# Kernel tuning notes

Hardware: AMD Instinct MI355X
Metric: run time of the kernel (lower is better)

Reference implementation:

```python
import jax, jax.numpy as jnp
import numpy as np

N_CLASSES = 12
IMG_SIZE = 512
BATCH = 8

CURV_MAX = jnp.array([1.2261, 1.1558, 1.1161, 1.1195, 2.7202, 2.3714,
                      1.7055, 3.2717, 2.6716, 5.0418, 0.4293], dtype=jnp.float32)


def setup_inputs() -> dict:
    key = jax.random.key(0)
    soft_anatomy = jax.random.normal(key, (BATCH, N_CLASSES, IMG_SIZE, IMG_SIZE), dtype=jnp.float32)
    return {"soft_anatomy": soft_anatomy}


def reference(soft_anatomy):
    nc1 = N_CLASSES - 1  # 11 layer channels
    pred_mask = soft_anatomy[:, :nc1]                      # [B, 11, H, W]
    sm = jax.nn.softmax(pred_mask, axis=2)                 # softmax over height (dim 2)
    lsm = jax.nn.log_softmax(pred_mask, axis=2)
    B, C, H, W = sm.shape

    # position mask: row index broadcast over width/channels
    pos = jnp.arange(H, dtype=sm.dtype)[None, None, :, None]  # [1,1,H,1]

    # expected layer position per column: [B, 11, W]
    layer_positions = jnp.sum(sm * pos, axis=2)

    # std deviations around layer positions: [B, 11, W]
    std_deviations = jnp.sqrt(
        jnp.sum(sm * (pos - layer_positions[:, :, None, :]) ** 2, axis=2))

    # topology violations between adjacent layers: [B, 10, W]
    topology_violations = jax.nn.relu(layer_positions[:, :-1] - layer_positions[:, 1:])

    # neighbour (continuity) diff along width: [B, 11, W-1]
    continuity_violations = jnp.abs(
        (jnp.roll(layer_positions, 1, axis=2) - layer_positions)[..., 1:])

    # curvature via depthwise conv1d with sobel [-1,0..0,1] and laplace [1,0..0,-2,0..0,1]
    # (kernel length 11, replicate pad 5 -> same width). torch conv1d is cross-correlation:
    #   first[w]  = -x[w] + x[w+10]
    #   second[w] =  x[w] - 2*x[w+5] + x[w+10]
    PAD = 5
    lpp = jnp.pad(layer_positions, ((0, 0), (0, 0), (PAD, PAD)), mode='edge')
    first_order = lpp[..., 10:] - lpp[..., :-10]
    second_order = lpp[..., :-10] - 2.0 * lpp[..., 5:-5] + lpp[..., 10:]
    curvature = second_order / jnp.power(1.0 + first_order ** 2, 1.5)
    curvature_diffs = jnp.abs(curvature) - CURV_MAX[None, :, None]  # curv_max broadcast over W

    # topological_engine_1d: new[i] = max(new[i-1], lp[i]) == cumulative max over class dim
    correct_layer_positions = jax.lax.cummax(layer_positions, axis=1)

    # cumulative mask: ones channel + cumsum over height -> [B, 12, H, W]
    cum = jnp.cumsum(sm, axis=2)
    ones = jnp.ones((B, 1, H, W), dtype=sm.dtype)
    cm = jnp.concatenate([ones, cum], axis=1)

    # topological_engine_2d: y[idx] = relu(c[idx] + y[idx-1] - 1), idx = 2..n_classes-1
    def step(carry, c):
        y = jax.nn.relu(c + carry - 1.0)
        return y, y

    _, ys = jax.lax.scan(step, cm[:, 1], jnp.moveaxis(cm[:, 2:], 1, 0))
    top_correct = jnp.concatenate([cm[:, :2], jnp.moveaxis(ys, 0, 1)], axis=1)  # [B,12,H,W]

    # separate_masks: forward diff in place; last channel unchanged
    clean_masks = jnp.concatenate(
        [top_correct[:, :-1] - top_correct[:, 1:], top_correct[:, -1:]], axis=1)

    return (lsm, correct_layer_positions, clean_masks,
            std_deviations, topology_violations, continuity_violations, curvature_diffs)
```

## Files before the change

### kernel.cpp

```cpp
#include <hip/hip_runtime.h>

#define BB 8
#define NC 12
#define NC1 11
#define HH 512
#define WW 512
#define NG 64
#define GH 8

static constexpr size_t CH = (size_t)HH * WW;

static constexpr size_t OFF_LSM   = 0;
static constexpr size_t OFF_CLP   = (size_t)BB * NC1 * CH;
static constexpr size_t OFF_CLEAN = OFF_CLP + (size_t)BB * NC1 * WW;
static constexpr size_t OFF_STD   = OFF_CLEAN + (size_t)BB * NC * CH;
static constexpr size_t OFF_TOPO  = OFF_STD + (size_t)BB * NC1 * WW;
static constexpr size_t OFF_CONT  = OFF_TOPO + (size_t)BB * (NC1 - 1) * WW;
static constexpr size_t OFF_CURV  = OFF_CONT + (size_t)BB * NC1 * (WW - 1);

static constexpr size_t WS_BASE = 0;
static constexpr size_t WS_INV  = WS_BASE + (size_t)BB * NC1 * NG * WW;
static constexpr size_t WS_LOG  = WS_INV + (size_t)BB * NC1 * WW;
static constexpr size_t WS_LP   = WS_LOG + (size_t)BB * NC1 * WW;

__global__ __launch_bounds__(256) void ka_stats(const float* __restrict__ in,
                                                float* __restrict__ ws,
                                                float* __restrict__ out) {
    const int tx = threadIdx.x & 63;
    const int ty = threadIdx.x >> 6;
    const int wt = blockIdx.x;
    const int c  = blockIdx.y;
    const int b  = blockIdx.z;
    const int w  = wt * 128 + tx * 2;
    const int bc = b * NC1 + c;

    __shared__ float lE[NG][128];
    __shared__ float lP[4][128];
    __shared__ float lQ[4][128];

    const float* p = in + (size_t)(b * NC + c) * CH + (size_t)(ty * 128) * WW + w;
    float Px = 0.f, Py = 0.f, Qx = 0.f, Qy = 0.f;
    for (int gl = 0; gl < 16; ++gl) {
        float Ex = 0.f, Ey = 0.f, P8x = 0.f, P8y = 0.f, Q8x = 0.f, Q8y = 0.f;
        const float hbase = (float)(ty * 128 + gl * 8);
#pragma unroll
        for (int i = 0; i < GH; ++i) {
            float2 x = *(const float2*)(p + (size_t)(gl * 8 + i) * WW);
            float ex = expf(x.x), ey = expf(x.y);
            float h = hbase + (float)i;
            Ex += ex; Ey += ey;
            P8x += h * ex; P8y += h * ey;
            Q8x += h * h * ex; Q8y += h * h * ey;
        }
        *(float2*)&lE[ty * 16 + gl][tx * 2] = make_float2(Ex, Ey);
        Px += P8x; Py += P8y;
        Qx += Q8x; Qy += Q8y;
    }
    *(float2*)&lP[ty][tx * 2] = make_float2(Px, Py);
    *(float2*)&lQ[ty][tx * 2] = make_float2(Qx, Qy);
    __syncthreads();
    if (ty != 0) return;

    float Sx = 0.f, Sy = 0.f;
#pragma unroll
    for (int g = 0; g < NG; ++g) {
        float2 e = *(const float2*)&lE[g][tx * 2];
        Sx += e.x; Sy += e.y;
    }
    const float invx = 1.f / Sx, invy = 1.f / Sy;
    float rx = 0.f, ry = 0.f;
    float* bp = ws + WS_BASE + (size_t)bc * NG * WW + w;
#pragma unroll
    for (int g = 0; g < NG; ++g) {
        *(float2*)(bp + (size_t)g * WW) = make_float2(rx * invx, ry * invy);
        float2 e = *(const float2*)&lE[g][tx * 2];
        rx += e.x; ry += e.y;
    }
    float Ptx = lP[0][tx*2] + lP[1][tx*2] + lP[2][tx*2] + lP[3][tx*2];
    float Pty = lP[0][tx*2+1] + lP[1][tx*2+1] + lP[2][tx*2+1] + lP[3][tx*2+1];
    float Qtx = lQ[0][tx*2] + lQ[1][tx*2] + lQ[2][tx*2] + lQ[3][tx*2];
    float Qty = lQ[0][tx*2+1] + lQ[1][tx*2+1] + lQ[2][tx*2+1] + lQ[3][tx*2+1];
    float lpx = Ptx * invx, lpy = Pty * invy;
    float vx = Qtx * invx - lpx * lpx; if (vx < 0.f) vx = 0.f;
    float vy = Qty * invy - lpy * lpy; if (vy < 0.f) vy = 0.f;

    const size_t o = (size_t)bc * WW + w;
    *(float2*)(ws + WS_INV + o) = make_float2(invx, invy);
    *(float2*)(ws + WS_LOG + o) = make_float2(logf(Sx), logf(Sy));
    *(float2*)(ws + WS_LP + o)  = make_float2(lpx, lpy);
    *(float2*)(out + OFF_STD + o) = make_float2(sqrtf(vx), sqrtf(vy));
}

__global__ __launch_bounds__(256) void kb_emit(const float* __restrict__ in,
                                               const float* __restrict__ ws,
                                               float* __restrict__ out) {
    const int t = threadIdx.x;
    const int g = blockIdx.x;
    const int b = blockIdx.y;
    const int w = t * 2;

    float2 cum[NC1], inv[NC1], lgs[NC1];
#pragma unroll
    for (int c = 0; c < NC1; ++c) {
        const size_t bc = (size_t)(b * NC1 + c);
        cum[c] = *(const float2*)(ws + WS_BASE + (bc * NG + g) * WW + w);
        inv[c] = *(const float2*)(ws + WS_INV + bc * WW + w);
        lgs[c] = *(const float2*)(ws + WS_LOG + bc * WW + w);
    }
    const float* ip  = in + (size_t)b * NC * CH + (size_t)(g * GH) * WW + w;
    float* lsm = out + OFF_LSM + (size_t)b * NC1 * CH + (size_t)(g * GH) * WW + w;
    float* cln = out + OFF_CLEAN + (size_t)b * NC * CH + (size_t)(g * GH) * WW + w;

    for (int i = 0; i < GH; ++i) {
        const size_t ho = (size_t)i * WW;
        float2 x[NC1];
#pragma unroll
        for (int c = 0; c < NC1; ++c)
            x[c] = *(const float2*)(ip + (size_t)c * CH + ho);
#pragma unroll
        for (int c = 0; c < NC1; ++c) {
            cum[c].x += expf(x[c].x) * inv[c].x;
            cum[c].y += expf(x[c].y) * inv[c].y;
            *(float2*)(lsm + (size_t)c * CH + ho) =
                make_float2(x[c].x - lgs[c].x, x[c].y - lgs[c].y);
        }
        float2 tc = cum[0];
        *(float2*)(cln + ho) = make_float2(1.f - tc.x, 1.f - tc.y);
#pragma unroll
        for (int k = 1; k < NC1; ++k) {
            float2 t2 = make_float2(fmaxf(cum[k].x + tc.x - 1.f, 0.f),
                                    fmaxf(cum[k].y + tc.y - 1.f, 0.f));
            *(float2*)(cln + (size_t)k * CH + ho) = make_float2(tc.x - t2.x, tc.y - t2.y);
            tc = t2;
        }
        *(float2*)(cln + (size_t)NC1 * CH + ho) = tc;
    }

    if (g != 0) return;
    const float CM[NC1] = {1.2261f, 1.1558f, 1.1161f, 1.1195f, 2.7202f, 2.3714f,
                           1.7055f, 3.2717f, 2.6716f, 5.0418f, 0.4293f};
    const float* lp = ws + WS_LP;
#pragma unroll
    for (int s = 0; s < 2; ++s) {
        const int wv = w + s;
        const int wm = (wv - 5 < 0) ? 0 : wv - 5;
        const int wp = (wv + 5 > WW - 1) ? WW - 1 : wv + 5;
        float m = 0.f, prev = 0.f;
        for (int c = 0; c < NC1; ++c) {
            const size_t rb = (size_t)(b * NC1 + c) * WW;
            const float lv = lp[rb + wv];
            m = (c == 0) ? lv : fmaxf(m, lv);
            out[OFF_CLP + rb + wv] = m;
            if (c > 0)
                out[OFF_TOPO + (size_t)(b * (NC1 - 1) + (c - 1)) * WW + wv] =
                    fmaxf(prev - lv, 0.f);
            prev = lv;
            if (wv < WW - 1) {
                const float nxt = lp[rb + wv + 1];
                out[OFF_CONT + (size_t)(b * NC1 + c) * (WW - 1) + wv] = fabsf(lv - nxt);
            }
            const float a  = lp[rb + wm];
            const float bb = lp[rb + wp];
            const float fo = bb - a;
            const float so = a - 2.f * lv + bb;
            const float bs = 1.f + fo * fo;
            out[OFF_CURV + rb + wv] = fabsf(so / (bs * sqrtf(bs))) - CM[c];
        }
    }
}

extern "C" void kernel_launch(void* const* d_in, const int* in_sizes, int n_in,
                              void* d_out, int out_size, void* d_ws, size_t ws_size,
                              hipStream_t stream) {
    const float* in = (const float*)d_in[0];
    float* out = (float*)d_out;
    float* ws = (float*)d_ws;

    hipLaunchKernelGGL(ka_stats, dim3(4, NC1, BB), dim3(256), 0, stream, in, ws, out);
    hipLaunchKernelGGL(kb_emit, dim3(NG, BB), dim3(256), 0, stream, in, ws, out);
}
```

Measured before the change: 83.54 us.

## Stage full column in LDS to emit log-softmax in stats pass, clean reads lsm

The stats kernel now loads an entire 512-row by 32-column tile into shared memory, computes the softmax stats, and writes log-softmax directly from LDS, so the input is read from global memory only once. The second kernel no longer reads the input. It reconstructs softmax as exp of the stored log-softmax and builds the clean masks from 32 chunk prefix offsets. This removes one full input read but adds a read-back of the lsm output, plus a 68KB LDS footprint per block that limits occupancy.

```diff
diff --git a/kernel.cpp b/kernel.cpp
--- a/kernel.cpp
+++ b/kernel.cpp
@@ -5,8 +5,10 @@
 #define NC1 11
 #define HH 512
 #define WW 512
-#define NG 64
-#define GH 8
+#define NCH 32
+#define HC 16
+#define WT 32
+#define XLD 34
 
 static constexpr size_t CH = (size_t)HH * WW;
 
@@ -19,153 +21,158 @@
 static constexpr size_t OFF_CURV  = OFF_CONT + (size_t)BB * NC1 * (WW - 1);
 
 static constexpr size_t WS_BASE = 0;
-static constexpr size_t WS_INV  = WS_BASE + (size_t)BB * NC1 * NG * WW;
-static constexpr size_t WS_LOG  = WS_INV + (size_t)BB * NC1 * WW;
-static constexpr size_t WS_LP   = WS_LOG + (size_t)BB * NC1 * WW;
+static constexpr size_t WS_LP   = WS_BASE + (size_t)BB * NC1 * NCH * WW;
 
-__global__ __launch_bounds__(256) void ka_stats(const float* __restrict__ in,
+__global__ __launch_bounds__(512) void ks_stats(const float* __restrict__ in,
                                                 float* __restrict__ ws,
                                                 float* __restrict__ out) {
-    const int tx = threadIdx.x & 63;
-    const int ty = threadIdx.x >> 6;
-    const int wt = blockIdx.x;
-    const int c  = blockIdx.y;
-    const int b  = blockIdx.z;
-    const int w  = wt * 128 + tx * 2;
+    const int t  = threadIdx.x;
+    const int wt = blockIdx.x, c = blockIdx.y, b = blockIdx.z;
     const int bc = b * NC1 + c;
+    const int w0 = wt * WT;
 
-    __shared__ float lE[NG][128];
-    __shared__ float lP[4][128];
-    __shared__ float lQ[4][128];
+    __shared__ float xs[HH][XLD];
+    __shared__ float cs[NCH][WT];
+    __shared__ float pP[16][WT];
+    __shared__ float pQ[16][WT];
+    __shared__ float lgS[WT];
 
-    const float* p = in + (size_t)(b * NC + c) * CH + (size_t)(ty * 128) * WW + w;
-    float Px = 0.f, Py = 0.f, Qx = 0.f, Qy = 0.f;
-    for (int gl = 0; gl < 16; ++gl) {
-        float Ex = 0.f, Ey = 0.f, P8x = 0.f, P8y = 0.f, Q8x = 0.f, Q8y = 0.f;
-        const float hbase = (float)(ty * 128 + gl * 8);
+    {
+        const int w2 = t & 15, r = t >> 4;
+        const float* p = in + (size_t)(b * NC + c) * CH + (size_t)r * WW + w0 + 2 * w2;
 #pragma unroll
-        for (int i = 0; i < GH; ++i) {
-            float2 x = *(const float2*)(p + (size_t)(gl * 8 + i) * WW);
-            float ex = expf(x.x), ey = expf(x.y);
-            float h = hbase + (float)i;
-            Ex += ex; Ey += ey;
-            P8x += h * ex; P8y += h * ey;
-            Q8x += h * h * ex; Q8y += h * h * ey;
+        for (int i = 0; i < 16; ++i) {
+            float2 v = *(const float2*)(p + (size_t)(i * 32) * WW);
+            xs[r + 32 * i][2 * w2]     = v.x;
+            xs[r + 32 * i][2 * w2 + 1] = v.y;
         }
-        *(float2*)&lE[ty * 16 + gl][tx * 2] = make_float2(Ex, Ey);
-        Px += P8x; Py += P8y;
-        Qx += Q8x; Qy += Q8y;
     }
-    *(float2*)&lP[ty][tx * 2] = make_float2(Px, Py);
-    *(float2*)&lQ[ty][tx * 2] = make_float2(Qx, Qy);
     __syncthreads();
-    if (ty != 0) return;
 
-    float Sx = 0.f, Sy = 0.f;
+    {
+        const int w = t & 31, q = t >> 5;
+        float P = 0.f, Q = 0.f;
 #pragma unroll
-    for (int g = 0; g < NG; ++g) {
-        float2 e = *(const float2*)&lE[g][tx * 2];
-        Sx += e.x; Sy += e.y;
+        for (int j = 0; j < 2; ++j) {
+            float E = 0.f;
+#pragma unroll
+            for (int i = 0; i < HC; ++i) {
+                const int h = q * 32 + j * HC + i;
+                const float e = expf(xs[h][w]);
+                const float hf = (float)h;
+                E += e; P += hf * e; Q += hf * hf * e;
+            }
+            cs[q * 2 + j][w] = E;
+        }
+        pP[q][w] = P; pQ[q][w] = Q;
     }
-    const float invx = 1.f / Sx, invy = 1.f / Sy;
-    float rx = 0.f, ry = 0.f;
-    float* bp = ws + WS_BASE + (size_t)bc * NG * WW + w;
+    __syncthreads();
+
+    if (t < WT) {
+        const int w = t;
+        float S = 0.f;
 #pragma unroll
-    for (int g = 0; g < NG; ++g) {
-        *(float2*)(bp + (size_t)g * WW) = make_float2(rx * invx, ry * invy);
-        float2 e = *(const float2*)&lE[g][tx * 2];
-        rx += e.x; ry += e.y;
+        for (int ch = 0; ch < NCH; ++ch) S += cs[ch][w];
+        const float inv = 1.f / S;
+        float run = 0.f;
+#pragma unroll
+        for (int ch = 0; ch < NCH; ++ch) {
+            const float e = cs[ch][w];
+            cs[ch][w] = run * inv;
+            run += e;
+        }
+        float P = 0.f, Q = 0.f;
+#pragma unroll
+        for (int q = 0; q < 16; ++q) { P += pP[q][w]; Q += pQ[q][w]; }
+        const float lp = P * inv;
+        float var = Q * inv - lp * lp; if (var < 0.f) var = 0.f;
+        lgS[w] = logf(S);
+        const size_t o = (size_t)bc * WW + w0 + w;
+        ws[WS_LP + o] = lp;
+        out[OFF_STD + o] = sqrtf(var);
     }
-    float Ptx = lP[0][tx*2] + lP[1][tx*2] + lP[2][tx*2] + lP[3][tx*2];
-    float Pty = lP[0][tx*2+1] + lP[1][tx*2+1] + lP[2][tx*2+1] + lP[3][tx*2+1];
-    float Qtx = lQ[0][tx*2] + lQ[1][tx*2] + lQ[2][tx*2] + lQ[3][tx*2];
-    float Qty = lQ[0][tx*2+1] + lQ[1][tx*2+1] + lQ[2][tx*2+1] + lQ[3][tx*2+1];
-    float lpx = Ptx * invx, lpy = Pty * invy;
-    float vx = Qtx * invx - lpx * lpx; if (vx < 0.f) vx = 0.f;
-    float vy = Qty * invy - lpy * lpy; if (vy < 0.f) vy = 0.f;
+    __syncthreads();
 
-    const size_t o = (size_t)bc * WW + w;
-    *(float2*)(ws + WS_INV + o) = make_float2(invx, invy);
-    *(float2*)(ws + WS_LOG + o) = make_float2(logf(Sx), logf(Sy));
-    *(float2*)(ws + WS_LP + o)  = make_float2(lpx, lpy);
-    *(float2*)(out + OFF_STD + o) = make_float2(sqrtf(vx), sqrtf(vy));
+    {
+        const int w = t & 31, chg = t >> 5;
+#pragma unroll
+        for (int j = 0; j < 2; ++j) {
+            const int ch = chg * 2 + j;
+            ws[WS_BASE + ((size_t)bc * NCH + ch) * WW + w0 + w] = cs[ch][w];
+        }
+    }
+    {
+        const int w2 = t & 15, r = t >> 4;
+        const float l0 = lgS[2 * w2], l1 = lgS[2 * w2 + 1];
+        float* lo = out + OFF_LSM + (size_t)bc * CH + (size_t)r * WW + w0 + 2 * w2;
+#pragma unroll
+        for (int i = 0; i < 16; ++i) {
+            const int h = r + 32 * i;
+            float2 v = make_float2(xs[h][2 * w2] - l0, xs[h][2 * w2 + 1] - l1);
+            *(float2*)(lo + (size_t)(i * 32) * WW) = v;
+        }
+    }
 }
 
-__global__ __launch_bounds__(256) void kb_emit(const float* __restrict__ in,
-                                               const float* __restrict__ ws,
-                                               float* __restrict__ out) {
+__global__ __launch_bounds__(256) void kc_clean(const float* __restrict__ ws,
+                                                float* __restrict__ out) {
     const int t = threadIdx.x;
-    const int g = blockIdx.x;
-    const int b = blockIdx.y;
-    const int w = t * 2;
+    const int wh = blockIdx.x, chunk = blockIdx.y, b = blockIdx.z;
+    const int w = wh * 256 + t;
 
-    float2 cum[NC1], inv[NC1], lgs[NC1];
+    float cum[NC1];
 #pragma unroll
-    for (int c = 0; c < NC1; ++c) {
-        const size_t bc = (size_t)(b * NC1 + c);
-        cum[c] = *(const float2*)(ws + WS_BASE + (bc * NG + g) * WW + w);
-        inv[c] = *(const float2*)(ws + WS_INV + bc * WW + w);
-        lgs[c] = *(const float2*)(ws + WS_LOG + bc * WW + w);
-    }
-    const float* ip  = in + (size_t)b * NC * CH + (size_t)(g * GH) * WW + w;
-    float* lsm = out + OFF_LSM + (size_t)b * NC1 * CH + (size_t)(g * GH) * WW + w;
-    float* cln = out + OFF_CLEAN + (size_t)b * NC * CH + (size_t)(g * GH) * WW + w;
+    for (int c = 0; c < NC1; ++c)
+        cum[c] = ws[WS_BASE + (((size_t)(b * NC1 + c)) * NCH + chunk) * WW + w];
 
-    for (int i = 0; i < GH; ++i) {
+    const float* lsm = out + OFF_LSM + (size_t)b * NC1 * CH + (size_t)(chunk * HC) * WW + w;
+    float* cln = out + OFF_CLEAN + (size_t)b * NC * CH + (size_t)(chunk * HC) * WW + w;
+
+    for (int i = 0; i < HC; ++i) {
         const size_t ho = (size_t)i * WW;
-        float2 x[NC1];
+        float s[NC1];
 #pragma unroll
         for (int c = 0; c < NC1; ++c)
-            x[c] = *(const float2*)(ip + (size_t)c * CH + ho);
+            s[c] = expf(lsm[(size_t)c * CH + ho]);
 #pragma unroll
-        for (int c = 0; c < NC1; ++c) {
-            cum[c].x += expf(x[c].x) * inv[c].x;
-            cum[c].y += expf(x[c].y) * inv[c].y;
-            *(float2*)(lsm + (size_t)c * CH + ho) =
-                make_float2(x[c].x - lgs[c].x, x[c].y - lgs[c].y);
-        }
-        float2 tc = cum[0];
-        *(float2*)(cln + ho) = make_float2(1.f - tc.x, 1.f - tc.y);
+        for (int c = 0; c < NC1; ++c)
+            cum[c] += s[c];
+        float tc = cum[0];
+        cln[ho] = 1.f - tc;
 #pragma unroll
         for (int k = 1; k < NC1; ++k) {
-            float2 t2 = make_float2(fmaxf(cum[k].x + tc.x - 1.f, 0.f),
-                                    fmaxf(cum[k].y + tc.y - 1.f, 0.f));
-            *(float2*)(cln + (size_t)k * CH + ho) = make_float2(tc.x - t2.x, tc.y - t2.y);
+            const float t2 = fmaxf(cum[k] + tc - 1.f, 0.f);
+            cln[(size_t)k * CH + ho] = tc - t2;
             tc = t2;
         }
-        *(float2*)(cln + (size_t)NC1 * CH + ho) = tc;
+        cln[(size_t)NC1 * CH + ho] = tc;
     }
 
-    if (g != 0) return;
+    if (chunk != 0) return;
     const float CM[NC1] = {1.2261f, 1.1558f, 1.1161f, 1.1195f, 2.7202f, 2.3714f,
                            1.7055f, 3.2717f, 2.6716f, 5.0418f, 0.4293f};
     const float* lp = ws + WS_LP;
-#pragma unroll
-    for (int s = 0; s < 2; ++s) {
-        const int wv = w + s;
-        const int wm = (wv - 5 < 0) ? 0 : wv - 5;
-        const int wp = (wv + 5 > WW - 1) ? WW - 1 : wv + 5;
-        float m = 0.f, prev = 0.f;
-        for (int c = 0; c < NC1; ++c) {
-            const size_t rb = (size_t)(b * NC1 + c) * WW;
-            const float lv = lp[rb + wv];
-            m = (c == 0) ? lv : fmaxf(m, lv);
-            out[OFF_CLP + rb + wv] = m;
-            if (c > 0)
-                out[OFF_TOPO + (size_t)(b * (NC1 - 1) + (c - 1)) * WW + wv] =
-                    fmaxf(prev - lv, 0.f);
-            prev = lv;
-            if (wv < WW - 1) {
-                const float nxt = lp[rb + wv + 1];
-                out[OFF_CONT + (size_t)(b * NC1 + c) * (WW - 1) + wv] = fabsf(lv - nxt);
-            }
-            const float a  = lp[rb + wm];
-            const float bb = lp[rb + wp];
-            const float fo = bb - a;
-            const float so = a - 2.f * lv + bb;
-            const float bs = 1.f + fo * fo;
-            out[OFF_CURV + rb + wv] = fabsf(so / (bs * sqrtf(bs))) - CM[c];
+    const int wm = (w - 5 < 0) ? 0 : w - 5;
+    const int wp = (w + 5 > WW - 1) ? WW - 1 : w + 5;
+    float m = 0.f, prev = 0.f;
+    for (int c = 0; c < NC1; ++c) {
+        const size_t rb = (size_t)(b * NC1 + c) * WW;
+        const float lv = lp[rb + w];
+        m = (c == 0) ? lv : fmaxf(m, lv);
+        out[OFF_CLP + rb + w] = m;
+        if (c > 0)
+            out[OFF_TOPO + (size_t)(b * (NC1 - 1) + (c - 1)) * WW + w] = fmaxf(prev - lv, 0.f);
+        prev = lv;
+        if (w < WW - 1) {
+            const float nxt = lp[rb + w + 1];
+            out[OFF_CONT + (size_t)(b * NC1 + c) * (WW - 1) + w] = fabsf(lv - nxt);
         }
+        const float a  = lp[rb + wm];
+        const float bb = lp[rb + wp];
+        const float fo = bb - a;
+        const float so = a - 2.f * lv + bb;
+        const float bs = 1.f + fo * fo;
+        out[OFF_CURV + rb + w] = fabsf(so / (bs * sqrtf(bs))) - CM[c];
     }
 }
 
@@ -176,6 +183,6 @@
     float* out = (float*)d_out;
     float* ws = (float*)d_ws;
 
-    hipLaunchKernelGGL(ka_stats, dim3(4, NC1, BB), dim3(256), 0, stream, in, ws, out);
-    hipLaunchKernelGGL(kb_emit, dim3(NG, BB), dim3(256), 0, stream, in, ws, out);
+    hipLaunchKernelGGL(ks_stats, dim3(16, NC1, BB), dim3(512), 0, stream, in, ws, out);
+    hipLaunchKernelGGL(kc_clean, dim3(2, NCH, BB), dim3(256), 0, stream, ws, out);
 }
```

Result: faster. 81.31 us (-2.7%).

## Widen stats kernel parallelism and compute softmax via exp of log-softmax

Applied to the files above, without the earlier changes.

The stats kernel now runs 512-thread blocks over 64-column tiles, with one column per thread and eight height slices, which doubles the grid and the threads per block. Prefix sums are normalized in shared memory and then written out by all threads with coalesced stores, instead of by a single wave. The emit kernel drops the separate inverse-sum buffer and gets softmax as exp of the log-softmax value, which removes one multiply and one workspace read per class. In exchange, stats loads become scalar rather than float2, and there is an extra block barrier.

```diff
diff --git a/kernel.cpp b/kernel.cpp
--- a/kernel.cpp
+++ b/kernel.cpp
@@ -19,76 +19,67 @@
 static constexpr size_t OFF_CURV  = OFF_CONT + (size_t)BB * NC1 * (WW - 1);
 
 static constexpr size_t WS_BASE = 0;
-static constexpr size_t WS_INV  = WS_BASE + (size_t)BB * NC1 * NG * WW;
-static constexpr size_t WS_LOG  = WS_INV + (size_t)BB * NC1 * WW;
+static constexpr size_t WS_LOG  = WS_BASE + (size_t)BB * NC1 * NG * WW;
 static constexpr size_t WS_LP   = WS_LOG + (size_t)BB * NC1 * WW;
 
-__global__ __launch_bounds__(256) void ka_stats(const float* __restrict__ in,
+__global__ __launch_bounds__(512) void ka_stats(const float* __restrict__ in,
                                                 float* __restrict__ ws,
                                                 float* __restrict__ out) {
-    const int tx = threadIdx.x & 63;
-    const int ty = threadIdx.x >> 6;
+    const int w = threadIdx.x & 63;
+    const int s = threadIdx.x >> 6;
     const int wt = blockIdx.x;
-    const int c  = blockIdx.y;
-    const int b  = blockIdx.z;
-    const int w  = wt * 128 + tx * 2;
+    const int c  = blockIdx.y, b = blockIdx.z;
     const int bc = b * NC1 + c;
+    const int w0 = wt * 64;
 
-    __shared__ float lE[NG][128];
-    __shared__ float lP[4][128];
-    __shared__ float lQ[4][128];
+    __shared__ float gE[NG][64];
+    __shared__ float gP[8][64];
+    __shared__ float gQ[8][64];
 
-    const float* p = in + (size_t)(b * NC + c) * CH + (size_t)(ty * 128) * WW + w;
-    float Px = 0.f, Py = 0.f, Qx = 0.f, Qy = 0.f;
-    for (int gl = 0; gl < 16; ++gl) {
-        float Ex = 0.f, Ey = 0.f, P8x = 0.f, P8y = 0.f, Q8x = 0.f, Q8y = 0.f;
-        const float hbase = (float)(ty * 128 + gl * 8);
+    const float* p = in + (size_t)(b * NC + c) * CH + (size_t)(s * 64) * WW + w0 + w;
+    float P = 0.f, Q = 0.f;
+#pragma unroll
+    for (int j = 0; j < 8; ++j) {
+        float E = 0.f;
 #pragma unroll
         for (int i = 0; i < GH; ++i) {
-            float2 x = *(const float2*)(p + (size_t)(gl * 8 + i) * WW);
-            float ex = expf(x.x), ey = expf(x.y);
-            float h = hbase + (float)i;
-            Ex += ex; Ey += ey;
-            P8x += h * ex; P8y += h * ey;
-            Q8x += h * h * ex; Q8y += h * h * ey;
+            const int h = s * 64 + j * GH + i;
+            const float e = expf(p[(size_t)(j * GH + i) * WW]);
+            const float hf = (float)h;
+            E += e; P += hf * e; Q += hf * hf * e;
         }
-        *(float2*)&lE[ty * 16 + gl][tx * 2] = make_float2(Ex, Ey);
-        Px += P8x; Py += P8y;
-        Qx += Q8x; Qy += Q8y;
+        gE[s * 8 + j][w] = E;
     }
-    *(float2*)&lP[ty][tx * 2] = make_float2(Px, Py);
-    *(float2*)&lQ[ty][tx * 2] = make_float2(Qx, Qy);
+    gP[s][w] = P; gQ[s][w] = Q;
     __syncthreads();
-    if (ty != 0) return;
 
-    float Sx = 0.f, Sy = 0.f;
+    if (threadIdx.x < 64) {
+        float S = 0.f;
 #pragma unroll
-    for (int g = 0; g < NG; ++g) {
-        float2 e = *(const float2*)&lE[g][tx * 2];
-        Sx += e.x; Sy += e.y;
+        for (int g = 0; g < NG; ++g) S += gE[g][w];
+        const float inv = 1.f / S;
+        float run = 0.f;
+#pragma unroll
+        for (int g = 0; g < NG; ++g) {
+            const float e = gE[g][w];
+            gE[g][w] = run * inv;
+            run += e;
+        }
+        float Pt = 0.f, Qt = 0.f;
+#pragma unroll
+        for (int s2 = 0; s2 < 8; ++s2) { Pt += gP[s2][w]; Qt += gQ[s2][w]; }
+        const float lp = Pt * inv;
+        float var = Qt * inv - lp * lp; if (var < 0.f) var = 0.f;
+        const size_t o = (size_t)bc * WW + w0 + w;
+        ws[WS_LOG + o] = logf(S);
+        ws[WS_LP + o]  = lp;
+        out[OFF_STD + o] = sqrtf(var);
     }
-    const float invx = 1.f / Sx, invy = 1.f / Sy;
-    float rx = 0.f, ry = 0.f;
-    float* bp = ws + WS_BASE + (size_t)bc * NG * WW + w;
+    __syncthreads();
+
 #pragma unroll
-    for (int g = 0; g < NG; ++g) {
-        *(float2*)(bp + (size_t)g * WW) = make_float2(rx * invx, ry * invy);
-        float2 e = *(const float2*)&lE[g][tx * 2];
-        rx += e.x; ry += e.y;
-    }
-    float Ptx = lP[0][tx*2] + lP[1][tx*2] + lP[2][tx*2] + lP[3][tx*2];
-    float Pty = lP[0][tx*2+1] + lP[1][tx*2+1] + lP[2][tx*2+1] + lP[3][tx*2+1];
-    float Qtx = lQ[0][tx*2] + lQ[1][tx*2] + lQ[2][tx*2] + lQ[3][tx*2];
-    float Qty = lQ[0][tx*2+1] + lQ[1][tx*2+1] + lQ[2][tx*2+1] + lQ[3][tx*2+1];
-    float lpx = Ptx * invx, lpy = Pty * invy;
-    float vx = Qtx * invx - lpx * lpx; if (vx < 0.f) vx = 0.f;
-    float vy = Qty * invy - lpy * lpy; if (vy < 0.f) vy = 0.f;
-
-    const size_t o = (size_t)bc * WW + w;
-    *(float2*)(ws + WS_INV + o) = make_float2(invx, invy);
-    *(float2*)(ws + WS_LOG + o) = make_float2(logf(Sx), logf(Sy));
-    *(float2*)(ws + WS_LP + o)  = make_float2(lpx, lpy);
-    *(float2*)(out + OFF_STD + o) = make_float2(sqrtf(vx), sqrtf(vy));
+    for (int j = 0; j < 8; ++j)
+        ws[WS_BASE + ((size_t)bc * NG + s * 8 + j) * WW + w0 + w] = gE[s * 8 + j][w];
 }
 
 __global__ __launch_bounds__(256) void kb_emit(const float* __restrict__ in,
@@ -99,12 +90,11 @@
     const int b = blockIdx.y;
     const int w = t * 2;
 
-    float2 cum[NC1], inv[NC1], lgs[NC1];
+    float2 cum[NC1], lgs[NC1];
 #pragma unroll
     for (int c = 0; c < NC1; ++c) {
         const size_t bc = (size_t)(b * NC1 + c);
         cum[c] = *(const float2*)(ws + WS_BASE + (bc * NG + g) * WW + w);
-        inv[c] = *(const float2*)(ws + WS_INV + bc * WW + w);
         lgs[c] = *(const float2*)(ws + WS_LOG + bc * WW + w);
     }
     const float* ip  = in + (size_t)b * NC * CH + (size_t)(g * GH) * WW + w;
@@ -119,17 +109,18 @@
             x[c] = *(const float2*)(ip + (size_t)c * CH + ho);
 #pragma unroll
         for (int c = 0; c < NC1; ++c) {
-            cum[c].x += expf(x[c].x) * inv[c].x;
-            cum[c].y += expf(x[c].y) * inv[c].y;
-            *(float2*)(lsm + (size_t)c * CH + ho) =
-                make_float2(x[c].x - lgs[c].x, x[c].y - lgs[c].y);
+            const float lx = x[c].x - lgs[c].x;
+            const float ly = x[c].y - lgs[c].y;
+            *(float2*)(lsm + (size_t)c * CH + ho) = make_float2(lx, ly);
+            cum[c].x += expf(lx);
+            cum[c].y += expf(ly);
         }
         float2 tc = cum[0];
         *(float2*)(cln + ho) = make_float2(1.f - tc.x, 1.f - tc.y);
 #pragma unroll
         for (int k = 1; k < NC1; ++k) {
-            float2 t2 = make_float2(fmaxf(cum[k].x + tc.x - 1.f, 0.f),
-                                    fmaxf(cum[k].y + tc.y - 1.f, 0.f));
+            const float2 t2 = make_float2(fmaxf(cum[k].x + tc.x - 1.f, 0.f),
+                                          fmaxf(cum[k].y + tc.y - 1.f, 0.f));
             *(float2*)(cln + (size_t)k * CH + ho) = make_float2(tc.x - t2.x, tc.y - t2.y);
             tc = t2;
         }
@@ -141,8 +132,8 @@
                            1.7055f, 3.2717f, 2.6716f, 5.0418f, 0.4293f};
     const float* lp = ws + WS_LP;
 #pragma unroll
-    for (int s = 0; s < 2; ++s) {
-        const int wv = w + s;
+    for (int sdx = 0; sdx < 2; ++sdx) {
+        const int wv = w + sdx;
         const int wm = (wv - 5 < 0) ? 0 : wv - 5;
         const int wp = (wv + 5 > WW - 1) ? WW - 1 : wv + 5;
         float m = 0.f, prev = 0.f;
@@ -176,6 +167,6 @@
     float* out = (float*)d_out;
     float* ws = (float*)d_ws;
 
-    hipLaunchKernelGGL(ka_stats, dim3(4, NC1, BB), dim3(256), 0, stream, in, ws, out);
+    hipLaunchKernelGGL(ka_stats, dim3(8, NC1, BB), dim3(512), 0, stream, in, ws, out);
     hipLaunchKernelGGL(kb_emit, dim3(NG, BB), dim3(256), 0, stream, in, ws, out);
 }
```

Measured after the change: 86.30 us. 1.03x slower.
